# Optimization experiments

Measured on AMD Instinct MI355X. Metric: run time of the kernel, lower is better.

The kernel has to match this reference:

```python
import jax, jax.numpy as jnp
import numpy as np

KSIZE = (15, 15)
SIGMA = (3.0, 3.0)


def _gaussian_kernel1d(kernel_size, sigma):
    ksize_half = (kernel_size - 1) * 0.5
    x = jnp.linspace(-ksize_half, ksize_half, kernel_size, dtype=jnp.float32)
    pdf = jnp.exp(-0.5 * (x / sigma) ** 2)
    return pdf / pdf.sum()


def setup_inputs() -> dict:
    key = jax.random.key(0)
    img = jax.random.normal(key, (8192, 8192), dtype=jnp.float32)
    # kernel = outer(kernel1d_y, kernel1d_x), matching torch.mm(y[:,None], x[None,:])
    k1d_x = _gaussian_kernel1d(KSIZE[0], SIGMA[0])
    k1d_y = _gaussian_kernel1d(KSIZE[1], SIGMA[1])
    kernel = jnp.outer(k1d_y, k1d_x)  # [kh, kw]
    return {"input": img, "kernel": kernel, "stride": 1}


def reference(input, kernel, stride):
    # forward(): squeeze -> custom mirror pad (== reflect, excludes edge) -> valid strided conv
    kh, kw = kernel.shape
    ph, pw = kh // 2, kw // 2
    x = jnp.pad(input, ((ph, ph), (pw, pw)), mode="reflect")  # matches the flip-based pad()
    # single-channel 2D cross-correlation, VALID padding, given stride
    out = jax.lax.conv_general_dilated(
        x[None, None, :, :],            # [1,1,H+2ph,W+2pw]
        kernel[None, None, :, :],       # [1,1,kh,kw]
        window_strides=(stride, stride),
        padding="VALID",
    )
    return out[0, 0]
```

## Files before the change

### kernel.cpp

```cpp
#include <hip/hip_runtime.h>

#define IMG_W 8192
#define IMG_H 8192
#define KS 15
#define RAD 7
#define TW 64
#define TH 64
#define BLOCK 256
#define SIN_W (TW + 2*RAD)
#define SIN_H (TH + 2*RAD)
#define SIN_STRIDE 80
#define MID_STRIDE TW

__device__ __forceinline__ int reflect_idx(int p, int n) {
    if (p < 0) p = -p;
    if (p >= n) p = 2 * n - 2 - p;
    return p;
}

__global__ __launch_bounds__(BLOCK)
void gauss15_fused(const float* __restrict__ in,
                   const float* __restrict__ k2d,
                   float* __restrict__ out) {
    __shared__ float s_in[SIN_H * SIN_STRIDE];
    __shared__ float s_mid[SIN_H * MID_STRIDE];
    __shared__ float s_kx[KS];
    __shared__ float s_ky[KS];

    const int t = threadIdx.x;
    const int col0 = blockIdx.x * TW;
    const int row0 = blockIdx.y * TH;

    if (t < KS) {
        float sx = 0.f, sy = 0.f;
        #pragma unroll
        for (int i = 0; i < KS; i++) {
            sx += k2d[i * KS + t];
            sy += k2d[t * KS + i];
        }
        s_kx[t] = sx;
        s_ky[t] = sy;
    }

    for (int idx = t; idx < SIN_H * SIN_W; idx += BLOCK) {
        int r = idx / SIN_W;
        int c = idx - r * SIN_W;
        int gr = reflect_idx(row0 - RAD + r, IMG_H);
        int gc = reflect_idx(col0 - RAD + c, IMG_W);
        s_in[r * SIN_STRIDE + c] = in[gr * IMG_W + gc];
    }
    __syncthreads();

    float kx[KS], ky[KS];
    #pragma unroll
    for (int i = 0; i < KS; i++) { kx[i] = s_kx[i]; ky[i] = s_ky[i]; }

    for (int idx = t; idx < SIN_H * (TW / 4); idx += BLOCK) {
        int r = idx >> 4;
        int cg = idx & 15;
        const float* rowp = &s_in[r * SIN_STRIDE + cg * 4];
        float f[20];
        *(float4*)(f + 0)  = *(const float4*)(rowp + 0);
        *(float4*)(f + 4)  = *(const float4*)(rowp + 4);
        *(float4*)(f + 8)  = *(const float4*)(rowp + 8);
        *(float4*)(f + 12) = *(const float4*)(rowp + 12);
        *(float4*)(f + 16) = *(const float4*)(rowp + 16);
        float a0 = 0.f, a1 = 0.f, a2 = 0.f, a3 = 0.f;
        #pragma unroll
        for (int j = 0; j < KS; j++) {
            float w = kx[j];
            a0 += f[j + 0] * w;
            a1 += f[j + 1] * w;
            a2 += f[j + 2] * w;
            a3 += f[j + 3] * w;
        }
        *(float4*)&s_mid[r * MID_STRIDE + cg * 4] = make_float4(a0, a1, a2, a3);
    }
    __syncthreads();

    const int cg = t & 15;
    const int rg = t >> 4;
    const int c = cg * 4;
    const int r0 = rg * 4;

    float4 acc[4];
    #pragma unroll
    for (int q = 0; q < 4; q++) acc[q] = make_float4(0.f, 0.f, 0.f, 0.f);

    #pragma unroll
    for (int i = 0; i < KS + 3; i++) {
        float4 v = *(const float4*)&s_mid[(r0 + i) * MID_STRIDE + c];
        #pragma unroll
        for (int q = 0; q < 4; q++) {
            int j = i - q;
            if (j >= 0 && j < KS) {
                float w = ky[j];
                acc[q].x += v.x * w;
                acc[q].y += v.y * w;
                acc[q].z += v.z * w;
                acc[q].w += v.w * w;
            }
        }
    }

    #pragma unroll
    for (int q = 0; q < 4; q++) {
        *(float4*)&out[(size_t)(row0 + r0 + q) * IMG_W + col0 + c] = acc[q];
    }
}

extern "C" void kernel_launch(void* const* d_in, const int* in_sizes, int n_in,
                              void* d_out, int out_size, void* d_ws, size_t ws_size,
                              hipStream_t stream) {
    const float* img = (const float*)d_in[0];
    const float* k2d = (const float*)d_in[1];
    float* out = (float*)d_out;

    dim3 grid(IMG_W / TW, IMG_H / TH);
    gauss15_fused<<<grid, BLOCK, 0, stream>>>(img, k2d, out);
}
```

Measured before the change: 517.1 us.

## Vectorize interior tile loads and widen horizontal pass to 16 outputs per thread

```diff
diff --git a/kernel.cpp b/kernel.cpp
--- a/kernel.cpp
+++ b/kernel.cpp
@@ -7,10 +7,9 @@
 #define TW 64
 #define TH 64
 #define BLOCK 256
-#define SIN_W (TW + 2*RAD)
-#define SIN_H (TH + 2*RAD)
+#define SROWS 78
 #define SIN_STRIDE 80
-#define MID_STRIDE TW
+#define MID_STRIDE 68
 
 __device__ __forceinline__ int reflect_idx(int p, int n) {
     if (p < 0) p = -p;
@@ -22,10 +21,9 @@
 void gauss15_fused(const float* __restrict__ in,
                    const float* __restrict__ k2d,
                    float* __restrict__ out) {
-    __shared__ float s_in[SIN_H * SIN_STRIDE];
-    __shared__ float s_mid[SIN_H * MID_STRIDE];
-    __shared__ float s_kx[KS];
-    __shared__ float s_ky[KS];
+    __shared__ float s_in[SROWS * SIN_STRIDE];
+    __shared__ float s_mid[SROWS * MID_STRIDE];
+    __shared__ float s_kx[KS], s_ky[KS];
 
     const int t = threadIdx.x;
     const int col0 = blockIdx.x * TW;
@@ -38,45 +36,63 @@
             sx += k2d[i * KS + t];
             sy += k2d[t * KS + i];
         }
-        s_kx[t] = sx;
-        s_ky[t] = sy;
+        s_kx[t] = sx; s_ky[t] = sy;
     }
 
-    for (int idx = t; idx < SIN_H * SIN_W; idx += BLOCK) {
-        int r = idx / SIN_W;
-        int c = idx - r * SIN_W;
-        int gr = reflect_idx(row0 - RAD + r, IMG_H);
-        int gc = reflect_idx(col0 - RAD + c, IMG_W);
-        s_in[r * SIN_STRIDE + c] = in[gr * IMG_W + gc];
+    const bool border = (blockIdx.x == 0) | (blockIdx.x == gridDim.x - 1) |
+                        (blockIdx.y == 0) | (blockIdx.y == gridDim.y - 1);
+
+    if (!border) {
+        for (int idx = t; idx < SROWS * 20; idx += BLOCK) {
+            int r = idx / 20;
+            int c4 = idx - r * 20;
+            const float4 v = *(const float4*)&in[(size_t)(row0 - RAD + r) * IMG_W
+                                                 + (col0 - 8 + c4 * 4)];
+            *(float4*)&s_in[r * SIN_STRIDE + c4 * 4] = v;
+        }
+    } else {
+        for (int idx = t; idx < SROWS * SIN_STRIDE; idx += BLOCK) {
+            int r = idx / SIN_STRIDE;
+            int c = idx - r * SIN_STRIDE;
+            int gr = reflect_idx(row0 - RAD + r, IMG_H);
+            int gc = reflect_idx(col0 - 8 + c, IMG_W);
+            s_in[r * SIN_STRIDE + c] = in[(size_t)gr * IMG_W + gc];
+        }
     }
     __syncthreads();
 
-    float kx[KS], ky[KS];
+    float kx[KS];
     #pragma unroll
-    for (int i = 0; i < KS; i++) { kx[i] = s_kx[i]; ky[i] = s_ky[i]; }
+    for (int i = 0; i < KS; i++) kx[i] = s_kx[i];
 
-    for (int idx = t; idx < SIN_H * (TW / 4); idx += BLOCK) {
-        int r = idx >> 4;
-        int cg = idx & 15;
-        const float* rowp = &s_in[r * SIN_STRIDE + cg * 4];
-        float f[20];
-        *(float4*)(f + 0)  = *(const float4*)(rowp + 0);
-        *(float4*)(f + 4)  = *(const float4*)(rowp + 4);
-        *(float4*)(f + 8)  = *(const float4*)(rowp + 8);
-        *(float4*)(f + 12) = *(const float4*)(rowp + 12);
-        *(float4*)(f + 16) = *(const float4*)(rowp + 16);
-        float a0 = 0.f, a1 = 0.f, a2 = 0.f, a3 = 0.f;
+    for (int tau = t; tau < SROWS * 4; tau += BLOCK) {
+        int r = tau >> 2;
+        int q = tau & 3;
+        const float* rowp = &s_in[r * SIN_STRIDE + q * 16];
+        float f[32];
+        #pragma unroll
+        for (int m = 0; m < 8; m++)
+            *(float4*)(f + 4 * m) = *(const float4*)(rowp + 4 * m);
+        float acc[16];
+        #pragma unroll
+        for (int k = 0; k < 16; k++) acc[k] = 0.f;
         #pragma unroll
         for (int j = 0; j < KS; j++) {
             float w = kx[j];
-            a0 += f[j + 0] * w;
-            a1 += f[j + 1] * w;
-            a2 += f[j + 2] * w;
-            a3 += f[j + 3] * w;
+            #pragma unroll
+            for (int k = 0; k < 16; k++)
+                acc[k] += f[k + 1 + j] * w;
         }
-        *(float4*)&s_mid[r * MID_STRIDE + cg * 4] = make_float4(a0, a1, a2, a3);
+        float* midp = &s_mid[r * MID_STRIDE + q * 16];
+        #pragma unroll
+        for (int m = 0; m < 4; m++)
+            *(float4*)(midp + 4 * m) = make_float4(acc[4*m], acc[4*m+1], acc[4*m+2], acc[4*m+3]);
     }
     __syncthreads();
+
+    float ky[KS];
+    #pragma unroll
+    for (int i = 0; i < KS; i++) ky[i] = s_ky[i];
 
     const int cg = t & 15;
     const int rg = t >> 4;
```

After: 561.7 us. 1.09x slower.
